# Performance work log

Hardware: AMD Instinct MI355X
Metric: run time of the kernel (lower is better)

## Reference

```python
import jax, jax.numpy as jnp
import numpy as np

B, S, D = 2, 4096, 2048
H = 16
HD = D // H          # head dim = 128
CHUNK = 64           # chunk size for O(N) chunked linear attention


def setup_inputs() -> dict:
    key = jax.random.key(0)
    ks = jax.random.split(key, 5)
    w = D ** -0.5  # fan-in init scale
    return {
        "x": jax.random.normal(ks[0], (B, S, D), jnp.float32),
        "Wq": jax.random.normal(ks[1], (D, D), jnp.float32) * w,
        "Wk": jax.random.normal(ks[2], (D, D), jnp.float32) * w,
        "Wv": jax.random.normal(ks[3], (D, D), jnp.float32) * w,
        "Wo": jax.random.normal(ks[4], (D, D), jnp.float32) * w,
    }


def _chunk_linear_attn(q, k, v):
    """Causal linear attention (identity feature map), chunked recurrent form.
    q, k, v: [b, h, n, d]. Equivalent to o_t = sum_{s<=t} (q_t . k_s) v_s.
    """
    b, h, n, d = q.shape
    nc = n // CHUNK
    q = q.reshape(b, h, nc, CHUNK, d)
    k = k.reshape(b, h, nc, CHUNK, d)
    v = v.reshape(b, h, nc, CHUNK, d)
    # intra-chunk causal part
    attn = jnp.einsum('bhncd,bhnsd->bhncs', q, k)
    causal = jnp.tril(jnp.ones((CHUNK, CHUNK), dtype=bool))
    attn = jnp.where(causal, attn, jnp.zeros((), attn.dtype))
    o_intra = jnp.einsum('bhncs,bhnsd->bhncd', attn, v)
    # inter-chunk recurrent state: S_i = sum_{j < i} K_j^T V_j  ([d, d] per head)
    kv = jnp.einsum('bhnsd,bhnse->bhnde', k, v)
    S = jnp.cumsum(kv, axis=2) - kv  # exclusive prefix sum over chunks
    o_inter = jnp.einsum('bhncd,bhnde->bhnce', q, S)
    return (o_intra + o_inter).reshape(b, h, n, d)


def reference(x, Wq, Wk, Wv, Wo):
    # bias-free projections (nn.Linear convention: y = x @ W.T)
    q = (x @ Wq.T).reshape(B, S, H, HD).transpose(0, 2, 1, 3)
    k = (x @ Wk.T).reshape(B, S, H, HD).transpose(0, 2, 1, 3)
    v = (x @ Wv.T).reshape(B, S, H, HD).transpose(0, 2, 1, 3)
    scale = HD ** -0.5  # fla chunk_linear_attn default scale on q
    o = _chunk_linear_attn(q * scale, k, v)
    o = o.transpose(0, 2, 1, 3).reshape(B, S, D)
    return o @ Wo.T
```

## Files before the change

kernel.cpp:

```cpp
#include <hip/hip_runtime.h>

typedef unsigned short u16;
typedef __attribute__((ext_vector_type(8))) short short8;
typedef __attribute__((ext_vector_type(8))) unsigned short u16x8;
typedef __attribute__((ext_vector_type(4))) unsigned short u16x4;
typedef __attribute__((ext_vector_type(2))) unsigned short u16x2;
typedef __attribute__((ext_vector_type(4))) float f32x4;

#define NBATCH 2
#define SEQ    4096
#define DIM    2048
#define NHEAD  16
#define HD     128
#define CH     64
#define NC     64
#define MROWS  8192

__device__ __forceinline__ float b2f(u16 u) {
    unsigned x = ((unsigned)u) << 16;
    return __builtin_bit_cast(float, x);
}
__device__ __forceinline__ u16 f2b(float f) {
    unsigned u = __builtin_bit_cast(unsigned, f);
    u += 0x7fffu + ((u >> 16) & 1u);
    return (u16)(u >> 16);
}

__device__ __forceinline__ void gload_lds16(const u16* g, u16* l) {
    __builtin_amdgcn_global_load_lds(
        (const __attribute__((address_space(1))) void*)g,
        (__attribute__((address_space(3))) void*)l, 16, 0, 0);
}

__global__ __launch_bounds__(256) void cast_all(
    const float* __restrict__ x,
    const float* __restrict__ w0, const float* __restrict__ w1,
    const float* __restrict__ w2, const float* __restrict__ w3,
    u16* __restrict__ xo,
    u16* __restrict__ o0, u16* __restrict__ o1,
    u16* __restrict__ o2, u16* __restrict__ o3)
{
    const int blk = blockIdx.x;
    const float* in;
    u16* out;
    long i;
    if (blk < 8192) {
        in = x; out = xo;
        i = (long)blk * 256 + threadIdx.x;
    } else {
        const int seg = (blk - 8192) >> 11;
        in  = seg == 0 ? w0 : seg == 1 ? w1 : seg == 2 ? w2 : w3;
        out = seg == 0 ? o0 : seg == 1 ? o1 : seg == 2 ? o2 : o3;
        i = (long)((blk - 8192) & 2047) * 256 + threadIdx.x;
    }
    f32x4 a = ((const f32x4*)in)[2 * i];
    f32x4 b = ((const f32x4*)in)[2 * i + 1];
    u16x8 o;
#pragma unroll
    for (int j = 0; j < 4; j++) { o[j] = f2b(a[j]); o[4 + j] = f2b(b[j]); }
    ((u16x8*)out)[i] = o;
}

#define BM 128
#define BN 128
#define BK 64

struct GemmCtx {
    int wave, lane, wr, wc, m16, quad;
    int row[4], koff[4], ldso[4];
    int fs0, fs1;
};

__device__ __forceinline__ GemmCtx gemm_ctx() {
    GemmCtx c;
    const int tid = threadIdx.x;
    c.wave = tid >> 6; c.lane = tid & 63;
    c.wr = c.wave >> 1; c.wc = c.wave & 1;
    c.m16 = c.lane & 15; c.quad = c.lane >> 4;
#pragma unroll
    for (int i = 0; i < 4; i++) {
        const int idx = c.wave * 64 + c.lane + 256 * i;
        const int row = idx >> 3, ps = idx & 7;
        c.row[i]  = row;
        c.koff[i] = (ps ^ (row & 7)) * 8;
        c.ldso[i] = idx * 8;
    }
    c.fs0 = ((0 + c.quad) ^ (c.m16 & 7)) * 8;
    c.fs1 = ((4 + c.quad) ^ (c.m16 & 7)) * 8;
    return c;
}

__device__ __forceinline__ void gemm_kloop(
    const GemmCtx& c, const u16* Ab, const u16* Bb, int K,
    u16* As, u16* Bs, f32x4 (&acc)[4][4])
{
    for (int kt = 0; kt < K; kt += BK) {
        if (kt) __syncthreads();
#pragma unroll
        for (int i = 0; i < 4; i++)
            gload_lds16(Ab + (long)c.row[i] * K + kt + c.koff[i], &As[c.ldso[i]]);
#pragma unroll
        for (int i = 0; i < 4; i++)
            gload_lds16(Bb + (long)c.row[i] * K + kt + c.koff[i], &Bs[c.ldso[i]]);
        __syncthreads();

#pragma unroll
        for (int kg = 0; kg < 2; kg++) {
            const int fs = kg ? c.fs1 : c.fs0;
            short8 af[4], bf[4];
#pragma unroll
            for (int t = 0; t < 4; t++)
                af[t] = *(const short8*)&As[(c.wr * 64 + t * 16 + c.m16) * BK + fs];
#pragma unroll
            for (int t = 0; t < 4; t++)
                bf[t] = *(const short8*)&Bs[(c.wc * 64 + t * 16 + c.m16) * BK + fs];
#pragma unroll
            for (int i = 0; i < 4; i++)
#pragma unroll
                for (int j = 0; j < 4; j++)
                    acc[i][j] = __builtin_amdgcn_mfma_f32_16x16x32_bf16(
                        af[i], bf[j], acc[i][j], 0, 0, 0);
        }
    }
}

__global__ __launch_bounds__(256) void gemm_qkv(
    const u16* __restrict__ A,
    const u16* __restrict__ Wqb, const u16* __restrict__ Wkb, const u16* __restrict__ Wvb,
    u16* __restrict__ q, u16* __restrict__ k, u16* __restrict__ kt,
    u16* __restrict__ vt, float qscale)
{
    __shared__ __align__(16) u16 As[BM * BK];
    __shared__ __align__(16) u16 Bs[BN * BK];
    const GemmCtx c = gemm_ctx();

    const int w = blockIdx.y >> 4;
    const long row0 = (long)blockIdx.x * BM;
    const long col0 = (long)(blockIdx.y & 15) * BN;
    const u16* Bw = w == 0 ? Wqb : w == 1 ? Wkb : Wvb;

    f32x4 acc[4][4];
#pragma unroll
    for (int i = 0; i < 4; i++)
#pragma unroll
        for (int j = 0; j < 4; j++) {
            f32x4 z = {0.f, 0.f, 0.f, 0.f};
            acc[i][j] = z;
        }

    gemm_kloop(c, A + row0 * DIM, Bw + col0 * DIM, DIM, As, Bs, acc);

    const float scale = (w == 0) ? qscale : 1.0f;
#pragma unroll
    for (int i = 0; i < 4; i++) {
        const long grow0 = row0 + c.wr * 64 + i * 16 + c.quad * 4;
#pragma unroll
        for (int j = 0; j < 4; j++) {
            const long gcol = col0 + c.wc * 64 + j * 16 + c.m16;
            u16x4 p;
#pragma unroll
            for (int r = 0; r < 4; r++) p[r] = f2b(acc[i][j][r] * scale);
            if (w == 0) {
#pragma unroll
                for (int r = 0; r < 4; r++) q[(grow0 + r) * DIM + gcol] = p[r];
            } else {
                const long b = grow0 >> 12;
                const long t0 = grow0 & (SEQ - 1);
                u16* Ct = (w == 1) ? kt : vt;
                *(u16x4*)(Ct + (b * DIM + gcol) * SEQ + t0) = p;
                if (w == 1) {
#pragma unroll
                    for (int r = 0; r < 4; r++) k[(grow0 + r) * DIM + gcol] = p[r];
                }
            }
        }
    }
}

__global__ __launch_bounds__(256) void gemm_out(
    const u16* __restrict__ A, const u16* __restrict__ Bw, float* __restrict__ C)
{
    __shared__ __align__(16) u16 As[BM * BK];
    __shared__ __align__(16) u16 Bs[BN * BK];
    const GemmCtx c = gemm_ctx();
    const long row0 = (long)blockIdx.x * BM;
    const long col0 = (long)blockIdx.y * BN;

    f32x4 acc[4][4];
#pragma unroll
    for (int i = 0; i < 4; i++)
#pragma unroll
        for (int j = 0; j < 4; j++) {
            f32x4 z = {0.f, 0.f, 0.f, 0.f};
            acc[i][j] = z;
        }

    gemm_kloop(c, A + row0 * DIM, Bw + col0 * DIM, DIM, As, Bs, acc);

#pragma unroll
    for (int i = 0; i < 4; i++) {
        const long grow0 = row0 + c.wr * 64 + i * 16 + c.quad * 4;
#pragma unroll
        for (int j = 0; j < 4; j++) {
            const long gcol = col0 + c.wc * 64 + j * 16 + c.m16;
#pragma unroll
            for (int r = 0; r < 4; r++)
                C[(grow0 + r) * DIM + gcol] = acc[i][j][r];
        }
    }
}

__global__ __launch_bounds__(256) void chunk_kv_mfma(
    const u16* __restrict__ Vt, const u16* __restrict__ Kt, u16* __restrict__ KV)
{
    const int tid = threadIdx.x, blk = blockIdx.x;
    const int c = blk & (NC - 1), bh = blk >> 6;
    const int wave = tid >> 6, lane = tid & 63;
    const int wr = wave >> 1, wc = wave & 1;
    const int m16 = lane & 15, quad = lane >> 4;
    const u16* vb = Vt + (long)bh * HD * SEQ + c * CH;
    const u16* kb = Kt + (long)bh * HD * SEQ + c * CH;

    f32x4 acc[4][4];
#pragma unroll
    for (int i = 0; i < 4; i++)
#pragma unroll
        for (int j = 0; j < 4; j++) {
            f32x4 z = {0.f, 0.f, 0.f, 0.f};
            acc[i][j] = z;
        }

#pragma unroll
    for (int tk = 0; tk < 2; tk++) {
        short8 af[4], bf[4];
#pragma unroll
        for (int t = 0; t < 4; t++)
            af[t] = *(const short8*)(vb + (long)(wr * 64 + t * 16 + m16) * SEQ + tk * 32 + quad * 8);
#pragma unroll
        for (int t = 0; t < 4; t++)
            bf[t] = *(const short8*)(kb + (long)(wc * 64 + t * 16 + m16) * SEQ + tk * 32 + quad * 8);
#pragma unroll
        for (int i = 0; i < 4; i++)
#pragma unroll
            for (int j = 0; j < 4; j++)
                acc[i][j] = __builtin_amdgcn_mfma_f32_16x16x32_bf16(
                    af[i], bf[j], acc[i][j], 0, 0, 0);
    }

    u16* outp = KV + (long)blk * (HD * HD);
#pragma unroll
    for (int i = 0; i < 4; i++)
#pragma unroll
        for (int j = 0; j < 4; j++)
#pragma unroll
            for (int r = 0; r < 4; r++)
                outp[(wr * 64 + i * 16 + quad * 4 + r) * HD + wc * 64 + j * 16 + m16]
                    = f2b(acc[i][j][r]);
}

__global__ __launch_bounds__(256) void kv_prefix(u16* __restrict__ KV)
{
    const int bh  = blockIdx.x >> 5;
    const int sub = blockIdx.x & 31;
    const long base = (long)bh * NC * (HD * HD) + (sub * 256 + threadIdx.x) * 2;
    float s0 = 0.f, s1 = 0.f;
#pragma unroll 4
    for (int c = 0; c < NC; c++) {
        u16* p = KV + base + (long)c * (HD * HD);
        u16x2 v = *(u16x2*)p;
        u16x2 w; w[0] = f2b(s0); w[1] = f2b(s1);
        *(u16x2*)p = w;
        s0 += b2f(v[0]); s1 += b2f(v[1]);
    }
}

#define AMP 72

__global__ __launch_bounds__(256) void chunk_out_mfma(
    const u16* __restrict__ Q, const u16* __restrict__ Kn,
    const u16* __restrict__ Vt, const u16* __restrict__ Sb, u16* __restrict__ O)
{
    __shared__ __align__(16) u16 Am[CH * AMP];

    const int tid = threadIdx.x, blk = blockIdx.x;
    const int c = blk & (NC - 1), bh = blk >> 6;
    const int h = bh & (NHEAD - 1), b = bh >> 4;
    const long rowbase = (long)b * SEQ + (long)c * CH;
    const int wave = tid >> 6, lane = tid & 63;
    const int m16 = lane & 15, quad = lane >> 4;

    const u16* qrow = Q  + (rowbase + wave * 16 + m16) * DIM + h * HD;
    const u16* krow = Kn + rowbase * DIM + h * HD;

    short8 qa[4];
#pragma unroll
    for (int dk = 0; dk < 4; dk++)
        qa[dk] = *(const short8*)(qrow + dk * 32 + quad * 8);

    f32x4 acc1[4];
#pragma unroll
    for (int jt = 0; jt < 4; jt++) {
        f32x4 z = {0.f, 0.f, 0.f, 0.f};
        acc1[jt] = z;
    }
#pragma unroll
    for (int dk = 0; dk < 4; dk++)
#pragma unroll
        for (int jt = 0; jt < 4; jt++) {
            short8 bb = *(const short8*)(krow + (long)(jt * 16 + m16) * DIM + dk * 32 + quad * 8);
            acc1[jt] = __builtin_amdgcn_mfma_f32_16x16x32_bf16(qa[dk], bb, acc1[jt], 0, 0, 0);
        }
    const int mbase = wave * 16 + quad * 4;
#pragma unroll
    for (int jt = 0; jt < 4; jt++) {
        const int j = jt * 16 + m16;
#pragma unroll
        for (int r = 0; r < 4; r++) {
            float v = (j <= mbase + r) ? acc1[jt][r] : 0.f;
            Am[(mbase + r) * AMP + j] = f2b(v);
        }
    }

    f32x4 acc[8];
#pragma unroll
    for (int et = 0; et < 8; et++) {
        f32x4 z = {0.f, 0.f, 0.f, 0.f};
        acc[et] = z;
    }
    const u16* Sg = Sb + (long)blk * (HD * HD);
#pragma unroll
    for (int dk = 0; dk < 4; dk++)
#pragma unroll
        for (int et = 0; et < 8; et++) {
            short8 sb = *(const short8*)(Sg + (et * 16 + m16) * HD + dk * 32 + quad * 8);
            acc[et] = __builtin_amdgcn_mfma_f32_16x16x32_bf16(qa[dk], sb, acc[et], 0, 0, 0);
        }

    const u16* vb = Vt + (long)bh * HD * SEQ + c * CH;
#pragma unroll
    for (int tk = 0; tk < 2; tk++) {
        short8 a = *(const short8*)&Am[(wave * 16 + m16) * AMP + tk * 32 + quad * 8];
#pragma unroll
        for (int et = 0; et < 8; et++) {
            short8 vbf = *(const short8*)(vb + (long)(et * 16 + m16) * SEQ + tk * 32 + quad * 8);
            acc[et] = __builtin_amdgcn_mfma_f32_16x16x32_bf16(a, vbf, acc[et], 0, 0, 0);
        }
    }

#pragma unroll
    for (int et = 0; et < 8; et++) {
        const int e = et * 16 + m16;
#pragma unroll
        for (int r = 0; r < 4; r++) {
            const int m = wave * 16 + quad * 4 + r;
            O[(rowbase + m) * DIM + h * HD + e] = f2b(acc[et][r]);
        }
    }
}

extern "C" void kernel_launch(void* const* d_in, const int* in_sizes, int n_in,
                              void* d_out, int out_size, void* d_ws, size_t ws_size,
                              hipStream_t stream)
{
    (void)in_sizes; (void)n_in; (void)out_size; (void)ws_size;
    const float* x  = (const float*)d_in[0];
    const float* Wq = (const float*)d_in[1];
    const float* Wk = (const float*)d_in[2];
    const float* Wv = (const float*)d_in[3];
    const float* Wo = (const float*)d_in[4];
    float* out = (float*)d_out;

    const long NE = (long)MROWS * DIM;
    const long WE = (long)DIM * DIM;
    u16* xb  = (u16*)d_ws;
    u16* Wqb = xb  + NE;
    u16* Wkb = Wqb + WE;
    u16* Wvb = Wkb + WE;
    u16* Wob = Wvb + WE;
    u16* q   = Wob + WE;
    u16* k   = q + NE;
    u16* vt  = k + NE;
    u16* kv  = vt + NE;
    u16* o   = xb;
    u16* kt  = (u16*)d_out;

    hipLaunchKernelGGL(cast_all, dim3(16384), dim3(256), 0, stream,
                       x, Wq, Wk, Wv, Wo, xb, Wqb, Wkb, Wvb, Wob);

    const float qscale = 0.08838834764831845f;

    hipLaunchKernelGGL(gemm_qkv, dim3(MROWS / BM, 48), dim3(256), 0, stream,
                       xb, Wqb, Wkb, Wvb, q, k, kt, vt, qscale);

    hipLaunchKernelGGL(chunk_kv_mfma, dim3(NBATCH * NHEAD * NC), dim3(256), 0, stream, vt, kt, kv);
    hipLaunchKernelGGL(kv_prefix,     dim3(1024),                dim3(256), 0, stream, kv);
    hipLaunchKernelGGL(chunk_out_mfma,dim3(NBATCH * NHEAD * NC), dim3(256), 0, stream, q, k, vt, kv, o);

    hipLaunchKernelGGL(gemm_out, dim3(MROWS / BM, DIM / BN), dim3(256), 0, stream, o, Wob, out);
}
```

Baseline: 597.5 us.

## Rewrite projection GEMMs with 256x256 tiles and 4-stage async LDS pipeline

Replaces the 128x128x64 single-buffered GEMM loop used by the QKV and output projections with a 256x256x32 tile, 8 waves per block, and a 4-deep ring of LDS buffers. Global-to-LDS loads for future K-steps are issued between MFMA batches, with vmcnt waits and s_setprio raised around the MFMAs. The goal is to hide memory latency and raise arithmetic intensity per block. It costs a larger accumulator register footprint and more LDS per block (128 KB), and the grid shrinks to fewer, larger blocks. A __syncthreads is also added in chunk_out_mfma before the V pass.

Result: faster. 553.5 us (-7.4%).

```diff
diff --git a/kernel.cpp b/kernel.cpp
--- a/kernel.cpp
+++ b/kernel.cpp
@@ -61,99 +61,159 @@
     ((u16x8*)out)[i] = o;
 }
 
-#define BM 128
-#define BN 128
-#define BK 64
-
-struct GemmCtx {
+#define GBM 256
+#define GBN 256
+#define GBK 32
+#define BUFE 16384
+
+struct Ctx8 {
     int wave, lane, wr, wc, m16, quad;
-    int row[4], koff[4], ldso[4];
-    int fs0, fs1;
+    int fl;
+    long grA[2];
+    int ldso[2];
 };
 
-__device__ __forceinline__ GemmCtx gemm_ctx() {
-    GemmCtx c;
+__device__ __forceinline__ Ctx8 ctx8(int K) {
+    Ctx8 c;
     const int tid = threadIdx.x;
     c.wave = tid >> 6; c.lane = tid & 63;
-    c.wr = c.wave >> 1; c.wc = c.wave & 1;
-    c.m16 = c.lane & 15; c.quad = c.lane >> 4;
-#pragma unroll
-    for (int i = 0; i < 4; i++) {
-        const int idx = c.wave * 64 + c.lane + 256 * i;
-        const int row = idx >> 3, ps = idx & 7;
-        c.row[i]  = row;
-        c.koff[i] = (ps ^ (row & 7)) * 8;
-        c.ldso[i] = idx * 8;
-    }
-    c.fs0 = ((0 + c.quad) ^ (c.m16 & 7)) * 8;
-    c.fs1 = ((4 + c.quad) ^ (c.m16 & 7)) * 8;
+    c.wr = c.wave >> 2; c.wc = c.wave & 3;
+    c.m16 = c.lane & 15; c.quad = (c.lane >> 4) & 3;
+    const int t3 = c.lane >> 3;
+    const int u3 = (c.lane & 7) ^ t3;
+    const int ml = 2 * t3 + (u3 >> 2);
+    const int sl = (u3 & 3) * 8;
+#pragma unroll
+    for (int i = 0; i < 2; i++) {
+        const int bi = 2 * c.wave + i;
+        c.grA[i] = (long)(bi * 16 + ml) * K + sl;
+        c.ldso[i] = bi * 512 + c.lane * 8;
+    }
+    const int line = c.m16 >> 1;
+    c.fl = line * 64 + ((((c.m16 & 1) << 2) | c.quad) ^ line) * 8;
     return c;
 }
 
-__device__ __forceinline__ void gemm_kloop(
-    const GemmCtx& c, const u16* Ab, const u16* Bb, int K,
-    u16* As, u16* Bs, f32x4 (&acc)[4][4])
-{
-    for (int kt = 0; kt < K; kt += BK) {
-        if (kt) __syncthreads();
-#pragma unroll
-        for (int i = 0; i < 4; i++)
-            gload_lds16(Ab + (long)c.row[i] * K + kt + c.koff[i], &As[c.ldso[i]]);
-#pragma unroll
-        for (int i = 0; i < 4; i++)
-            gload_lds16(Bb + (long)c.row[i] * K + kt + c.koff[i], &Bs[c.ldso[i]]);
-        __syncthreads();
-
-#pragma unroll
-        for (int kg = 0; kg < 2; kg++) {
-            const int fs = kg ? c.fs1 : c.fs0;
-            short8 af[4], bf[4];
-#pragma unroll
-            for (int t = 0; t < 4; t++)
-                af[t] = *(const short8*)&As[(c.wr * 64 + t * 16 + c.m16) * BK + fs];
-#pragma unroll
-            for (int t = 0; t < 4; t++)
-                bf[t] = *(const short8*)&Bs[(c.wc * 64 + t * 16 + c.m16) * BK + fs];
-#pragma unroll
-            for (int i = 0; i < 4; i++)
-#pragma unroll
-                for (int j = 0; j < 4; j++)
-                    acc[i][j] = __builtin_amdgcn_mfma_f32_16x16x32_bf16(
-                        af[i], bf[j], acc[i][j], 0, 0, 0);
-        }
-    }
-}
-
-__global__ __launch_bounds__(256) void gemm_qkv(
+template<bool STG>
+__device__ __forceinline__ void tile8(
+    const Ctx8& c, const u16* As, const u16* Bs, f32x4 (&acc)[8][4],
+    const u16* pA, const u16* pB, long ktN, u16* AsN, u16* BsN)
+{
+    short8 af[4], bf[4];
+#pragma unroll
+    for (int t = 0; t < 4; t++)
+        af[t] = *(const short8*)&As[(c.wr * 8 + t) * 512 + c.fl];
+#pragma unroll
+    for (int t = 0; t < 4; t++)
+        bf[t] = *(const short8*)&Bs[(c.wc * 4 + t) * 512 + c.fl];
+    if (STG) {
+        gload_lds16(pA + c.grA[0] + ktN, AsN + c.ldso[0]);
+        gload_lds16(pA + c.grA[1] + ktN, AsN + c.ldso[1]);
+    }
+    __builtin_amdgcn_s_setprio(1);
+#pragma unroll
+    for (int i = 0; i < 4; i++)
+#pragma unroll
+        for (int j = 0; j < 4; j++)
+            acc[i][j] = __builtin_amdgcn_mfma_f32_16x16x32_bf16(
+                af[i], bf[j], acc[i][j], 0, 0, 0);
+    __builtin_amdgcn_s_setprio(0);
+
+#pragma unroll
+    for (int t = 0; t < 4; t++)
+        af[t] = *(const short8*)&As[(c.wr * 8 + 4 + t) * 512 + c.fl];
+    if (STG) {
+        gload_lds16(pB + c.grA[0] + ktN, BsN + c.ldso[0]);
+        gload_lds16(pB + c.grA[1] + ktN, BsN + c.ldso[1]);
+    }
+    __builtin_amdgcn_s_setprio(1);
+#pragma unroll
+    for (int i = 0; i < 4; i++)
+#pragma unroll
+        for (int j = 0; j < 4; j++)
+            acc[4 + i][j] = __builtin_amdgcn_mfma_f32_16x16x32_bf16(
+                af[i], bf[j], acc[4 + i][j], 0, 0, 0);
+    __builtin_amdgcn_s_setprio(0);
+}
+
+__device__ __forceinline__ void kloop8(
+    const Ctx8& c, const u16* pA, const u16* pB, int K, u16* L, f32x4 (&acc)[8][4])
+{
+    const int NT = K >> 5;
+#pragma unroll
+    for (int t = 0; t < 3; t++) {
+        u16* As = L + t * BUFE;
+        u16* Bs = As + 8192;
+        gload_lds16(pA + c.grA[0] + t * GBK, As + c.ldso[0]);
+        gload_lds16(pA + c.grA[1] + t * GBK, As + c.ldso[1]);
+        gload_lds16(pB + c.grA[0] + t * GBK, Bs + c.ldso[0]);
+        gload_lds16(pB + c.grA[1] + t * GBK, Bs + c.ldso[1]);
+    }
+#pragma unroll 1
+    for (int u = 0; u < NT - 3; ++u) {
+        asm volatile("s_waitcnt vmcnt(8)" ::: "memory");
+        __builtin_amdgcn_s_barrier();
+        asm volatile("" ::: "memory");
+        u16* As  = L + (u & 3) * BUFE;
+        u16* AsN = L + ((u + 3) & 3) * BUFE;
+        tile8<true>(c, As, As + 8192, acc, pA, pB, (long)(u + 3) * GBK,
+                    AsN, AsN + 8192);
+    }
+    {
+        const int u = NT - 3;
+        asm volatile("s_waitcnt vmcnt(8)" ::: "memory");
+        __builtin_amdgcn_s_barrier();
+        asm volatile("" ::: "memory");
+        u16* As = L + (u & 3) * BUFE;
+        tile8<false>(c, As, As + 8192, acc, pA, pB, 0, nullptr, nullptr);
+    }
+    {
+        const int u = NT - 2;
+        asm volatile("s_waitcnt vmcnt(4)" ::: "memory");
+        __builtin_amdgcn_s_barrier();
+        asm volatile("" ::: "memory");
+        u16* As = L + (u & 3) * BUFE;
+        tile8<false>(c, As, As + 8192, acc, pA, pB, 0, nullptr, nullptr);
+    }
+    {
+        const int u = NT - 1;
+        asm volatile("s_waitcnt vmcnt(0)" ::: "memory");
+        __builtin_amdgcn_s_barrier();
+        asm volatile("" ::: "memory");
+        u16* As = L + (u & 3) * BUFE;
+        tile8<false>(c, As, As + 8192, acc, pA, pB, 0, nullptr, nullptr);
+    }
+}
+
+__global__ __launch_bounds__(512, 2) void gemm_qkv(
     const u16* __restrict__ A,
     const u16* __restrict__ Wqb, const u16* __restrict__ Wkb, const u16* __restrict__ Wvb,
     u16* __restrict__ q, u16* __restrict__ k, u16* __restrict__ kt,
     u16* __restrict__ vt, float qscale)
 {
-    __shared__ __align__(16) u16 As[BM * BK];
-    __shared__ __align__(16) u16 Bs[BN * BK];
-    const GemmCtx c = gemm_ctx();
-
-    const int w = blockIdx.y >> 4;
-    const long row0 = (long)blockIdx.x * BM;
-    const long col0 = (long)(blockIdx.y & 15) * BN;
+    __shared__ __align__(16) u16 L[4 * BUFE];
+    const Ctx8 c = ctx8(DIM);
+
+    const int w = blockIdx.y >> 3;
+    const long row0 = (long)blockIdx.x * GBM;
+    const long col0 = (long)(blockIdx.y & 7) * GBN;
     const u16* Bw = w == 0 ? Wqb : w == 1 ? Wkb : Wvb;
 
-    f32x4 acc[4][4];
-#pragma unroll
-    for (int i = 0; i < 4; i++)
+    f32x4 acc[8][4];
+#pragma unroll
+    for (int i = 0; i < 8; i++)
 #pragma unroll
         for (int j = 0; j < 4; j++) {
             f32x4 z = {0.f, 0.f, 0.f, 0.f};
             acc[i][j] = z;
         }
 
-    gemm_kloop(c, A + row0 * DIM, Bw + col0 * DIM, DIM, As, Bs, acc);
+    kloop8(c, A + row0 * DIM, Bw + col0 * DIM, DIM, L, acc);
 
     const float scale = (w == 0) ? qscale : 1.0f;
 #pragma unroll
-    for (int i = 0; i < 4; i++) {
-        const long grow0 = row0 + c.wr * 64 + i * 16 + c.quad * 4;
+    for (int i = 0; i < 8; i++) {
+        const long grow0 = row0 + c.wr * 128 + i * 16 + c.quad * 4;
 #pragma unroll
         for (int j = 0; j < 4; j++) {
             const long gcol = col0 + c.wc * 64 + j * 16 + c.m16;
@@ -177,29 +237,28 @@
     }
 }
 
-__global__ __launch_bounds__(256) void gemm_out(
+__global__ __launch_bounds__(512, 2) void gemm_out(
     const u16* __restrict__ A, const u16* __restrict__ Bw, float* __restrict__ C)
 {
-    __shared__ __align__(16) u16 As[BM * BK];
-    __shared__ __align__(16) u16 Bs[BN * BK];
-    const GemmCtx c = gemm_ctx();
-    const long row0 = (long)blockIdx.x * BM;
-    const long col0 = (long)blockIdx.y * BN;
-
-    f32x4 acc[4][4];
-#pragma unroll
-    for (int i = 0; i < 4; i++)
+    __shared__ __align__(16) u16 L[4 * BUFE];
+    const Ctx8 c = ctx8(DIM);
+    const long row0 = (long)blockIdx.x * GBM;
+    const long col0 = (long)blockIdx.y * GBN;
+
+    f32x4 acc[8][4];
+#pragma unroll
+    for (int i = 0; i < 8; i++)
 #pragma unroll
         for (int j = 0; j < 4; j++) {
             f32x4 z = {0.f, 0.f, 0.f, 0.f};
             acc[i][j] = z;
         }
 
-    gemm_kloop(c, A + row0 * DIM, Bw + col0 * DIM, DIM, As, Bs, acc);
-
-#pragma unroll
-    for (int i = 0; i < 4; i++) {
-        const long grow0 = row0 + c.wr * 64 + i * 16 + c.quad * 4;
+    kloop8(c, A + row0 * DIM, Bw + col0 * DIM, DIM, L, acc);
+
+#pragma unroll
+    for (int i = 0; i < 8; i++) {
+        const long grow0 = row0 + c.wr * 128 + i * 16 + c.quad * 4;
 #pragma unroll
         for (int j = 0; j < 4; j++) {
             const long gcol = col0 + c.wc * 64 + j * 16 + c.m16;
@@ -336,6 +395,7 @@
             acc[et] = __builtin_amdgcn_mfma_f32_16x16x32_bf16(qa[dk], sb, acc[et], 0, 0, 0);
         }
 
+    __syncthreads();
     const u16* vb = Vt + (long)bh * HD * SEQ + c * CH;
 #pragma unroll
     for (int tk = 0; tk < 2; tk++) {
@@ -389,12 +449,12 @@
 
     const float qscale = 0.08838834764831845f;
 
-    hipLaunchKernelGGL(gemm_qkv, dim3(MROWS / BM, 48), dim3(256), 0, stream,
+    hipLaunchKernelGGL(gemm_qkv, dim3(MROWS / GBM, 24), dim3(512), 0, stream,
                        xb, Wqb, Wkb, Wvb, q, k, kt, vt, qscale);
 
     hipLaunchKernelGGL(chunk_kv_mfma, dim3(NBATCH * NHEAD * NC), dim3(256), 0, stream, vt, kt, kv);
     hipLaunchKernelGGL(kv_prefix,     dim3(1024),                dim3(256), 0, stream, kv);
     hipLaunchKernelGGL(chunk_out_mfma,dim3(NBATCH * NHEAD * NC), dim3(256), 0, stream, q, k, vt, kv, o);
 
-    hipLaunchKernelGGL(gemm_out, dim3(MROWS / BM, DIM / BN), dim3(256), 0, stream, o, Wob, out);
-}
+    hipLaunchKernelGGL(gemm_out, dim3(MROWS / GBM, DIM / GBN), dim3(512), 0, stream, o, Wob, out);
+}
```
